# Performance work log

Hardware: AMD Instinct MI355X
Metric: run time of the kernel (lower is better)

## Reference

```python
import jax, jax.numpy as jnp
import numpy as np

N_QUBITS = 10
N_LAYERS = 3
OUT_MIN, OUT_MAX = -0.1, 0.1


def _apply_1q(state, U, wire):
    # state: (B, 2**n) complex64; U: (2,2) complex64 gate on `wire` (wire 0 = MSB, PennyLane order)
    B = state.shape[0]
    s = state.reshape(B, 2 ** wire, 2, -1)
    s = jnp.einsum('ij,bljr->blir', U, s)
    return s.reshape(B, -1)


def _apply_ry_batched(state, theta, wire):
    # per-sample RY(theta) on `wire`; theta: (B,)
    B = state.shape[0]
    s = state.reshape(B, 2 ** wire, 2, -1)
    c = jnp.cos(0.5 * theta)[:, None, None]
    si = jnp.sin(0.5 * theta)[:, None, None]
    a0, a1 = s[:, :, 0, :], s[:, :, 1, :]
    s = jnp.stack([c * a0 - si * a1, si * a0 + c * a1], axis=2)
    return s.reshape(B, -1)


def _apply_cnot(state, ctrl):
    # CNOT with control=ctrl, target=ctrl+1 (adjacent wires)
    B = state.shape[0]
    s = state.reshape(B, 2 ** ctrl, 2, 2, -1)
    s = jnp.stack([s[:, :, 0], s[:, :, 1, ::-1]], axis=2)
    return s.reshape(B, -1)


def _circuit(z, weights):
    # Faithful statevector simulation of the PennyLane qnode, batched over samples.
    B = z.shape[0]
    n = N_QUBITS
    state = jnp.zeros((B, 2 ** n), jnp.complex64).at[:, 0].set(1.0)
    zc = jnp.clip(z, -1.0, 1.0)
    for i in range(n):
        state = _apply_ry_batched(state, zc[:, i % zc.shape[1]], i)
    # Fuse RZ(a)->RY(b)->RZ(c) per (layer, qubit) into one 2x2 unitary: U = Rz(c) @ Ry(b) @ Rz(a)
    a, b, c = weights[..., 0], weights[..., 1], weights[..., 2]
    ea, eap = jnp.exp(-0.5j * a), jnp.exp(0.5j * a)
    ec, ecp = jnp.exp(-0.5j * c), jnp.exp(0.5j * c)
    cb, sb = jnp.cos(0.5 * b), jnp.sin(0.5 * b)
    U = jnp.stack([jnp.stack([ec * cb * ea, -ec * sb * eap], -1),
                   jnp.stack([ecp * sb * ea, ecp * cb * eap], -1)], -2)  # (L, Q, 2, 2)
    U = U.astype(jnp.complex64)
    for l in range(N_LAYERS):
        for i in range(n):
            state = _apply_1q(state, U[l, i], i)
        for i in range(n - 1):
            state = _apply_cnot(state, i)
    probs = jnp.abs(state) ** 2  # (B, 2**n) float32
    feats = []
    for i in range(n):
        p = probs.reshape(B, 2 ** i, 2, -1)
        feats.append(p[:, :, 0].sum((1, 2)) - p[:, :, 1].sum((1, 2)))  # <Z_i>
    return jnp.stack(feats, -1)  # (B, n_qubits)


def setup_inputs() -> dict:
    key = jax.random.key(0)
    ks = jax.random.split(key, 8)
    B = 4096
    return {
        'z': jax.random.normal(ks[0], (B, N_QUBITS), jnp.float32),
        'weights': jax.random.normal(ks[1], (N_LAYERS, N_QUBITS, 3), jnp.float32) * 0.01,
        'W1': jax.random.normal(ks[2], (N_QUBITS, 32), jnp.float32) * 0.3,
        'b1': jax.random.normal(ks[3], (32,), jnp.float32) * 0.05,
        'W2': jax.random.normal(ks[4], (32, 16), jnp.float32) * 0.2,
        'b2': jax.random.normal(ks[5], (16,), jnp.float32) * 0.05,
        'W3': jax.random.normal(ks[6], (16, 1), jnp.float32) * 0.2,
        'b3': jax.random.normal(ks[7], (1,), jnp.float32) * 0.05,
    }


def reference(z, weights, W1, b1, W2, b2, W3, b3):
    feats = _circuit(z, weights)                  # (B, n_qubits)
    h = jnp.tanh(feats @ W1 + b1)
    h = jnp.tanh(h @ W2 + b2)
    raw = h @ W3 + b3                             # (B, 1)
    return jax.nn.sigmoid(raw) * (OUT_MAX - OUT_MIN) + OUT_MIN
```

## Files before the change

kernel.cpp:

```cpp
#include <hip/hip_runtime.h>

namespace {

constexpr int NQ = 10;

struct cplx { float re, im; };

__device__ __forceinline__ cplx cmul(cplx a, cplx b) {
  return cplx{ fmaf(a.re, b.re, -a.im * b.im), fmaf(a.re, b.im, a.im * b.re) };
}
__device__ __forceinline__ cplx cmadd2(cplx u, cplx a, cplx v, cplx b) {
  cplx r;
  r.re = fmaf(u.re, a.re, fmaf(-u.im, a.im, fmaf(v.re, b.re, -v.im * b.im)));
  r.im = fmaf(u.re, a.im, fmaf( u.im, a.re, fmaf(v.re, b.im,  v.im * b.re)));
  return r;
}
__device__ __forceinline__ cplx csel(bool c, cplx x, cplx y) {
  return cplx{ c ? x.re : y.re, c ? x.im : y.im };
}

__device__ __forceinline__ float fast_tanh(float x) {
  float xc = fminf(fmaxf(x, -10.f), 10.f);
  float e = __expf(2.f * xc);
  return __fdividef(e - 1.f, e + 1.f);
}

__device__ __forceinline__ float rdlane(float v, int l) {
  return __int_as_float(__builtin_amdgcn_readlane(__float_as_int(v), l));
}
template<int CTRL>
__device__ __forceinline__ float dppf(float v) {
  return __int_as_float(__builtin_amdgcn_update_dpp(0, __float_as_int(v), CTRL, 0xF, 0xF, true));
}
template<int CTRL>
__device__ __forceinline__ cplx dppc(cplx v) { return cplx{ dppf<CTRL>(v.re), dppf<CTRL>(v.im) }; }

template<int PAT>
__device__ __forceinline__ float swzf(float v) {
  return __int_as_float(__builtin_amdgcn_ds_swizzle(__float_as_int(v), PAT));
}
__device__ __forceinline__ float bperm(int addr, float v) {
  return __int_as_float(__builtin_amdgcn_ds_bpermute(addr, __float_as_int(v)));
}

struct Umat { float r00,i00,r01,i01,r10,i10,r11,i11; };
__device__ __forceinline__ void getU(const Umat& m, int g,
                                     cplx& u00, cplx& u01, cplx& u10, cplx& u11) {
  u00 = cplx{rdlane(m.r00, g), rdlane(m.i00, g)};
  u01 = cplx{rdlane(m.r01, g), rdlane(m.i01, g)};
  u10 = cplx{rdlane(m.r10, g), rdlane(m.i10, g)};
  u11 = cplx{rdlane(m.r11, g), rdlane(m.i11, g)};
}

__device__ __forceinline__ void gate_lane_rt(cplx (&amp)[16], int lane, const Umat& m,
                                             int g, int LX, int HIL) {
  cplx u00, u01, u10, u11; getU(m, g, u00, u01, u10, u11);
  bool hi = (__popc(lane & HIL) & 1) != 0;
  cplx cA = csel(hi, u11, u00), cB = csel(hi, u10, u01);
  const int addr = (lane ^ LX) << 2;
  float ore[16], oim[16];
  #pragma unroll
  for (int t = 0; t < 16; ++t) { ore[t] = bperm(addr, amp[t].re); oim[t] = bperm(addr, amp[t].im); }
  #pragma unroll
  for (int t = 0; t < 16; ++t) amp[t] = cmadd2(cA, amp[t], cB, cplx{ore[t], oim[t]});
}

template<int CTRL, int LOCX, int HIL>
__device__ __forceinline__ void gate_mixed(cplx (&amp)[16], int lane, cplx u00,cplx u01,cplx u10,cplx u11) {
  bool hi = (__popc(lane & HIL) & 1) != 0;
  cplx cA = csel(hi, u11, u00), cB = csel(hi, u10, u01);
  #pragma unroll
  for (int t0 = 0; t0 < 16; ++t0) {
    if (t0 & LOCX) continue;
    const int t1 = t0 | LOCX;
    cplx o0 = dppc<CTRL>(amp[t1]);
    cplx o1 = dppc<CTRL>(amp[t0]);
    amp[t0] = cmadd2(cA, amp[t0], cB, o0);
    amp[t1] = cmadd2(cA, amp[t1], cB, o1);
  }
}
constexpr int hbit(int m) { return m >= 8 ? 8 : (m >= 4 ? 4 : (m >= 2 ? 2 : 1)); }
template<int PLOC, int HIL, int HILOC>
__device__ __forceinline__ void gate_local(cplx (&amp)[16], int lane, cplx u00,cplx u01,cplx u10,cplx u11) {
  bool h0 = (__popc(lane & HIL) & 1) != 0;
  cplx cA0 = csel(h0, u11, u00), cB0 = csel(h0, u10, u01);
  cplx cA1 = csel(h0, u00, u11), cB1 = csel(h0, u01, u10);
  #pragma unroll
  for (int ta = 0; ta < 16; ++ta) {
    if (ta & hbit(PLOC)) continue;
    const int tb = ta ^ PLOC;
    const bool pa = (__popc(ta & HILOC) & 1) != 0;
    cplx aA = amp[ta], aB = amp[tb];
    if (!pa) { amp[ta] = cmadd2(cA0, aA, cB0, aB); amp[tb] = cmadd2(cA1, aB, cB1, aA); }
    else     { amp[ta] = cmadd2(cA1, aA, cB1, aB); amp[tb] = cmadd2(cA0, aB, cB0, aA); }
  }
}

__device__ __forceinline__ float wht6(float v, float s1, float s2, float s4,
                                      float s8, float s16, float s32) {
  float o;
  o = dppf<0xB1>(v);               v = fmaf(s1,  v, o);
  o = dppf<0x4E>(v);               v = fmaf(s2,  v, o);
  o = dppf<0x1B>(dppf<0x141>(v));  v = fmaf(s4,  v, o);
  o = dppf<0x128>(v);              v = fmaf(s8,  v, o);
  o = swzf<0x401F>(v);             v = fmaf(s16, v, o);
  o = __shfl_xor(v, 32);           v = fmaf(s32, v, o);
  return v;
}

constexpr int pk6(int a, int b, int c, int d, int e) {
  return a | (b << 6) | (c << 12) | (d << 18) | (e << 24);
}
constexpr int LX1  = pk6(0x30, 0x18, 0x0C, 0x06, 0x03);
constexpr int HIL1 = pk6(0x20, 0x30, 0x38, 0x3C, 0x3E);
constexpr int LX2  = pk6(0x28, 0x14, 0x0A, 0x05, 0);
constexpr int HIL2 = pk6(0x20, 0x10, 0x28, 0x14, 0);

__global__ __launch_bounds__(64, 1)
void qgan_kernel(const float* __restrict__ z, const float* __restrict__ wts,
                 const float* __restrict__ W1, const float* __restrict__ b1,
                 const float* __restrict__ W2, const float* __restrict__ b2,
                 const float* __restrict__ W3, const float* __restrict__ b3,
                 float* __restrict__ out, int B)
{
  const int lane = threadIdx.x;
  const int wv   = blockIdx.x;
  if (wv >= B) return;

  const int j32 = lane & 31, k16 = lane & 15;
  float w1r[10];
  #pragma unroll
  for (int i = 0; i < NQ; ++i) w1r[i] = W1[i * 32 + j32];
  float b1v = b1[j32], b2v = b2[k16], w3v = W3[k16], b3v = b3[0];

  Umat m;
  {
    int g = (lane < 30) ? lane : 0;
    float wa = wts[g * 3 + 0], wb = wts[g * 3 + 1], wc = wts[g * 3 + 2];
    float al = 0.5f * (wa + wc), be = 0.5f * (wa - wc), hb = 0.5f * wb;
    float ca = __cosf(al),  sa = __sinf(al);
    float cbe = __cosf(be), sbe = __sinf(be);
    float cb = __cosf(hb),  sb = __sinf(hb);
    m.r00 =  cb * ca;  m.i00 = -cb * sa;
    m.r01 = -sb * cbe; m.i01 = -sb * sbe;
    m.r10 =  sb * cbe; m.i10 = -sb * sbe;
    m.r11 =  cb * ca;  m.i11 =  cb * sa;
  }

  cplx u00, u01, u10, u11;
  const float* zp = z + wv * NQ;

  cplx laneF = {1.f, 0.f};
  #pragma unroll
  for (int q = 0; q < 6; ++q) {
    float zz = fminf(fmaxf(zp[q], -1.f), 1.f);
    float c0 = __cosf(0.5f * zz), s0 = __sinf(0.5f * zz);
    getU(m, q, u00, u01, u10, u11);
    cplx va = { fmaf(u00.re, c0, u01.re * s0), fmaf(u00.im, c0, u01.im * s0) };
    cplx vb = { fmaf(u10.re, c0, u11.re * s0), fmaf(u10.im, c0, u11.im * s0) };
    cplx f = csel((lane >> (5 - q)) & 1, vb, va);
    laneF = (q == 0) ? f : cmul(laneF, f);
  }
  cplx va_[4], vb_[4];
  #pragma unroll
  for (int q = 6; q < 10; ++q) {
    float zz = fminf(fmaxf(zp[q], -1.f), 1.f);
    float c0 = __cosf(0.5f * zz), s0 = __sinf(0.5f * zz);
    getU(m, q, u00, u01, u10, u11);
    va_[q - 6] = { fmaf(u00.re, c0, u01.re * s0), fmaf(u00.im, c0, u01.im * s0) };
    vb_[q - 6] = { fmaf(u10.re, c0, u11.re * s0), fmaf(u10.im, c0, u11.im * s0) };
  }

  cplx amp[16];
  {
    cplx P2[4];
    P2[0] = cmul(va_[2], va_[3]);
    P2[1] = cmul(va_[2], vb_[3]);
    P2[2] = cmul(vb_[2], va_[3]);
    P2[3] = cmul(vb_[2], vb_[3]);
    cplx g0 = cmul(laneF, va_[0]);
    cplx g1 = cmul(laneF, vb_[0]);
    #pragma unroll
    for (int t = 0; t < 16; ++t) {
      cplx t7 = ((t >> 2) & 1) ? vb_[1] : va_[1];
      cplx tt = cmul(t7, P2[t & 3]);
      amp[t] = cmul(((t >> 3) & 1) ? g1 : g0, tt);
    }
  }

  #pragma unroll 1
  for (int i = 0; i < 5; ++i)
    gate_lane_rt(amp, lane, m, 10 + i, (LX1 >> (6 * i)) & 63, (HIL1 >> (6 * i)) & 63);
  getU(m, 15, u00,u01,u10,u11); gate_mixed<0xB1, 8, 0x3F>(amp, lane, u00,u01,u10,u11);
  getU(m, 16, u00,u01,u10,u11); gate_local<0xC, 0x3F, 0x8>(amp, lane, u00,u01,u10,u11);
  getU(m, 17, u00,u01,u10,u11); gate_local<0x6, 0x3F, 0xC>(amp, lane, u00,u01,u10,u11);
  getU(m, 18, u00,u01,u10,u11); gate_local<0x3, 0x3F, 0xE>(amp, lane, u00,u01,u10,u11);
  getU(m, 19, u00,u01,u10,u11); gate_local<0x1, 0x3F, 0xF>(amp, lane, u00,u01,u10,u11);

  #pragma unroll 1
  for (int i = 0; i < 4; ++i)
    gate_lane_rt(amp, lane, m, 20 + i, (LX2 >> (6 * i)) & 63, (HIL2 >> (6 * i)) & 63);
  getU(m, 24, u00,u01,u10,u11); gate_mixed<0x4E, 8, 0x2A>(amp, lane, u00,u01,u10,u11);
  getU(m, 25, u00,u01,u10,u11); gate_mixed<0xB1, 4, 0x15>(amp, lane, u00,u01,u10,u11);
  getU(m, 26, u00,u01,u10,u11); gate_local<0xA, 0x2A, 0x8>(amp, lane, u00,u01,u10,u11);
  getU(m, 27, u00,u01,u10,u11); gate_local<0x5, 0x15, 0x4>(amp, lane, u00,u01,u10,u11);
  getU(m, 28, u00,u01,u10,u11); gate_local<0x2, 0x2A, 0xA>(amp, lane, u00,u01,u10,u11);
  getU(m, 29, u00,u01,u10,u11); gate_local<0x1, 0x15, 0x5>(amp, lane, u00,u01,u10,u11);

  float p[16];
  #pragma unroll
  for (int t = 0; t < 16; ++t)
    p[t] = fmaf(amp[t].re, amp[t].re, amp[t].im * amp[t].im);

  #pragma unroll
  for (int k = 1; k <= 8; k <<= 1) {
    #pragma unroll
    for (int t = 0; t < 16; ++t) {
      if (t & k) continue;
      float a = p[t], b = p[t | k];
      p[t] = a + b; p[t | k] = a - b;
    }
  }

  float w2r[32];
  #pragma unroll
  for (int jj = 0; jj < 32; ++jj) w2r[jj] = W2[jj * 16 + k16];

  float s1  = (lane & 1)  ? -1.f : 1.f;
  float s2  = (lane & 2)  ? -1.f : 1.f;
  float s4  = (lane & 4)  ? -1.f : 1.f;
  float s8  = (lane & 8)  ? -1.f : 1.f;
  float s16 = (lane & 16) ? -1.f : 1.f;
  float s32 = (lane & 32) ? -1.f : 1.f;
  float B0 = wht6(p[0],   s1,s2,s4,s8,s16,s32);
  float B8 = wht6(p[8],   s1,s2,s4,s8,s16,s32);
  float BC = wht6(p[0xC], s1,s2,s4,s8,s16,s32);
  float B6 = wht6(p[6],   s1,s2,s4,s8,s16,s32);
  float B3 = wht6(p[3],   s1,s2,s4,s8,s16,s32);

  float feats[10];
  feats[0] = rdlane(B0, 0x20); feats[1] = rdlane(B0, 0x30);
  feats[2] = rdlane(B0, 0x18); feats[3] = rdlane(B0, 0x0C);
  feats[4] = rdlane(B0, 0x26); feats[5] = rdlane(B0, 0x33);
  feats[6] = rdlane(B8, 0x19); feats[7] = rdlane(BC, 0x0C);
  feats[8] = rdlane(B6, 0x26); feats[9] = rdlane(B3, 0x33);

  float acc = b1v;
  #pragma unroll
  for (int i = 0; i < NQ; ++i) acc = fmaf(feats[i], w1r[i], acc);
  float h1 = fast_tanh(acc);

  float acc2 = b2v;
  #pragma unroll
  for (int jj = 0; jj < 32; ++jj)
    acc2 = fmaf(rdlane(h1, jj), w2r[jj], acc2);
  float h2 = fast_tanh(acc2);

  float vv = h2 * w3v;
  vv += dppf<0xB1>(vv);
  vv += dppf<0x4E>(vv);
  vv += dppf<0x1B>(dppf<0x141>(vv));
  vv += dppf<0x128>(vv);

  if (lane == 0) out[wv] = 0.1f * fast_tanh(0.5f * (vv + b3v));
}

}

extern "C" void kernel_launch(void* const* d_in, const int* in_sizes, int n_in,
                              void* d_out, int out_size, void* d_ws, size_t ws_size,
                              hipStream_t stream) {
  const float* z   = (const float*)d_in[0];
  const float* wts = (const float*)d_in[1];
  const float* W1  = (const float*)d_in[2];
  const float* b1  = (const float*)d_in[3];
  const float* W2  = (const float*)d_in[4];
  const float* b2  = (const float*)d_in[5];
  const float* W3  = (const float*)d_in[6];
  const float* b3  = (const float*)d_in[7];
  float* out = (float*)d_out;
  (void)d_ws; (void)ws_size;

  int B = in_sizes[0] / NQ;
  hipLaunchKernelGGL(qgan_kernel, dim3(B), dim3(64), 0, stream,
                     z, wts, W1, b1, W2, b2, W3, b3, out, B);
}
```

Baseline: 90.94 us.

## Apply CNOT chains explicitly via bpermute and pack four waves per block

Replaces the earlier approach, which folded the CNOT chains into permuted gate indexing with parity selects, with an explicit CNOT-chain permutation per layer done through one bpermute pass plus a register reshuffle. Single-qubit gates become simple per-bit lane gates and local gates with no parity bookkeeping. The launch moves from one 64-thread block per sample to 256-thread blocks holding four samples, and the MLP weight loads are moved later to lower register pressure. This adds three cross-lane permutation passes but simplifies every gate and aims to improve occupancy and scheduling.

```diff
diff --git a/kernel.cpp b/kernel.cpp
--- a/kernel.cpp
+++ b/kernel.cpp
@@ -32,9 +32,6 @@
 __device__ __forceinline__ float dppf(float v) {
   return __int_as_float(__builtin_amdgcn_update_dpp(0, __float_as_int(v), CTRL, 0xF, 0xF, true));
 }
-template<int CTRL>
-__device__ __forceinline__ cplx dppc(cplx v) { return cplx{ dppf<CTRL>(v.re), dppf<CTRL>(v.im) }; }
-
 template<int PAT>
 __device__ __forceinline__ float swzf(float v) {
   return __int_as_float(__builtin_amdgcn_ds_swizzle(__float_as_int(v), PAT));
@@ -52,12 +49,12 @@
   u11 = cplx{rdlane(m.r11, g), rdlane(m.i11, g)};
 }
 
-__device__ __forceinline__ void gate_lane_rt(cplx (&amp)[16], int lane, const Umat& m,
-                                             int g, int LX, int HIL) {
+__device__ __forceinline__ void lane_gate(cplx (&amp)[16], int lane, const Umat& m,
+                                          int g, int kb) {
   cplx u00, u01, u10, u11; getU(m, g, u00, u01, u10, u11);
-  bool hi = (__popc(lane & HIL) & 1) != 0;
+  bool hi = ((lane >> kb) & 1) != 0;
   cplx cA = csel(hi, u11, u00), cB = csel(hi, u10, u01);
-  const int addr = (lane ^ LX) << 2;
+  const int addr = (lane ^ (1 << kb)) << 2;
   float ore[16], oim[16];
   #pragma unroll
   for (int t = 0; t < 16; ++t) { ore[t] = bperm(addr, amp[t].re); oim[t] = bperm(addr, amp[t].im); }
@@ -65,34 +62,31 @@
   for (int t = 0; t < 16; ++t) amp[t] = cmadd2(cA, amp[t], cB, cplx{ore[t], oim[t]});
 }
 
-template<int CTRL, int LOCX, int HIL>
-__device__ __forceinline__ void gate_mixed(cplx (&amp)[16], int lane, cplx u00,cplx u01,cplx u10,cplx u11) {
-  bool hi = (__popc(lane & HIL) & 1) != 0;
-  cplx cA = csel(hi, u11, u00), cB = csel(hi, u10, u01);
+template<int BBIT>
+__device__ __forceinline__ void local_gate(cplx (&amp)[16], const Umat& m, int g) {
+  cplx u00, u01, u10, u11; getU(m, g, u00, u01, u10, u11);
   #pragma unroll
   for (int t0 = 0; t0 < 16; ++t0) {
-    if (t0 & LOCX) continue;
-    const int t1 = t0 | LOCX;
-    cplx o0 = dppc<CTRL>(amp[t1]);
-    cplx o1 = dppc<CTRL>(amp[t0]);
-    amp[t0] = cmadd2(cA, amp[t0], cB, o0);
-    amp[t1] = cmadd2(cA, amp[t1], cB, o1);
-  }
-}
-constexpr int hbit(int m) { return m >= 8 ? 8 : (m >= 4 ? 4 : (m >= 2 ? 2 : 1)); }
-template<int PLOC, int HIL, int HILOC>
-__device__ __forceinline__ void gate_local(cplx (&amp)[16], int lane, cplx u00,cplx u01,cplx u10,cplx u11) {
-  bool h0 = (__popc(lane & HIL) & 1) != 0;
-  cplx cA0 = csel(h0, u11, u00), cB0 = csel(h0, u10, u01);
-  cplx cA1 = csel(h0, u00, u11), cB1 = csel(h0, u01, u10);
-  #pragma unroll
-  for (int ta = 0; ta < 16; ++ta) {
-    if (ta & hbit(PLOC)) continue;
-    const int tb = ta ^ PLOC;
-    const bool pa = (__popc(ta & HILOC) & 1) != 0;
-    cplx aA = amp[ta], aB = amp[tb];
-    if (!pa) { amp[ta] = cmadd2(cA0, aA, cB0, aB); amp[tb] = cmadd2(cA1, aB, cB1, aA); }
-    else     { amp[ta] = cmadd2(cA1, aA, cB1, aB); amp[tb] = cmadd2(cA0, aB, cB0, aA); }
+    if (t0 & BBIT) continue;
+    const int t1 = t0 | BBIT;
+    cplx a0 = amp[t0], a1 = amp[t1];
+    amp[t0] = cmadd2(u00, a0, u01, a1);
+    amp[t1] = cmadd2(u10, a0, u11, a1);
+  }
+}
+
+__device__ __forceinline__ void chain(cplx (&amp)[16], int lane) {
+  const int addr = ((lane ^ (lane >> 1)) & 63) << 2;
+  float ore[16], oim[16];
+  #pragma unroll
+  for (int t = 0; t < 16; ++t) { ore[t] = bperm(addr, amp[t].re); oim[t] = bperm(addr, amp[t].im); }
+  const bool ctrl = (lane & 1) != 0;
+  #pragma unroll
+  for (int t = 0; t < 16; ++t) {
+    const int ta = t ^ (t >> 1);
+    const int tb = ta ^ 8;
+    amp[t].re = ctrl ? ore[tb] : ore[ta];
+    amp[t].im = ctrl ? oim[tb] : oim[ta];
   }
 }
 
@@ -108,30 +102,17 @@
   return v;
 }
 
-constexpr int pk6(int a, int b, int c, int d, int e) {
-  return a | (b << 6) | (c << 12) | (d << 18) | (e << 24);
-}
-constexpr int LX1  = pk6(0x30, 0x18, 0x0C, 0x06, 0x03);
-constexpr int HIL1 = pk6(0x20, 0x30, 0x38, 0x3C, 0x3E);
-constexpr int LX2  = pk6(0x28, 0x14, 0x0A, 0x05, 0);
-constexpr int HIL2 = pk6(0x20, 0x10, 0x28, 0x14, 0);
-
-__global__ __launch_bounds__(64, 1)
+__global__ __launch_bounds__(256, 4)
 void qgan_kernel(const float* __restrict__ z, const float* __restrict__ wts,
                  const float* __restrict__ W1, const float* __restrict__ b1,
                  const float* __restrict__ W2, const float* __restrict__ b2,
                  const float* __restrict__ W3, const float* __restrict__ b3,
                  float* __restrict__ out, int B)
 {
-  const int lane = threadIdx.x;
-  const int wv   = blockIdx.x;
+  const int tid  = blockIdx.x * 256 + threadIdx.x;
+  const int lane = threadIdx.x & 63;
+  const int wv   = __builtin_amdgcn_readfirstlane(tid >> 6);
   if (wv >= B) return;
-
-  const int j32 = lane & 31, k16 = lane & 15;
-  float w1r[10];
-  #pragma unroll
-  for (int i = 0; i < NQ; ++i) w1r[i] = W1[i * 32 + j32];
-  float b1v = b1[j32], b2v = b2[k16], w3v = W3[k16], b3v = b3[0];
 
   Umat m;
   {
@@ -189,23 +170,19 @@
   }
 
   #pragma unroll 1
-  for (int i = 0; i < 5; ++i)
-    gate_lane_rt(amp, lane, m, 10 + i, (LX1 >> (6 * i)) & 63, (HIL1 >> (6 * i)) & 63);
-  getU(m, 15, u00,u01,u10,u11); gate_mixed<0xB1, 8, 0x3F>(amp, lane, u00,u01,u10,u11);
-  getU(m, 16, u00,u01,u10,u11); gate_local<0xC, 0x3F, 0x8>(amp, lane, u00,u01,u10,u11);
-  getU(m, 17, u00,u01,u10,u11); gate_local<0x6, 0x3F, 0xC>(amp, lane, u00,u01,u10,u11);
-  getU(m, 18, u00,u01,u10,u11); gate_local<0x3, 0x3F, 0xE>(amp, lane, u00,u01,u10,u11);
-  getU(m, 19, u00,u01,u10,u11); gate_local<0x1, 0x3F, 0xF>(amp, lane, u00,u01,u10,u11);
-
-  #pragma unroll 1
-  for (int i = 0; i < 4; ++i)
-    gate_lane_rt(amp, lane, m, 20 + i, (LX2 >> (6 * i)) & 63, (HIL2 >> (6 * i)) & 63);
-  getU(m, 24, u00,u01,u10,u11); gate_mixed<0x4E, 8, 0x2A>(amp, lane, u00,u01,u10,u11);
-  getU(m, 25, u00,u01,u10,u11); gate_mixed<0xB1, 4, 0x15>(amp, lane, u00,u01,u10,u11);
-  getU(m, 26, u00,u01,u10,u11); gate_local<0xA, 0x2A, 0x8>(amp, lane, u00,u01,u10,u11);
-  getU(m, 27, u00,u01,u10,u11); gate_local<0x5, 0x15, 0x4>(amp, lane, u00,u01,u10,u11);
-  getU(m, 28, u00,u01,u10,u11); gate_local<0x2, 0x2A, 0xA>(amp, lane, u00,u01,u10,u11);
-  getU(m, 29, u00,u01,u10,u11); gate_local<0x1, 0x15, 0x5>(amp, lane, u00,u01,u10,u11);
+  for (int l = 0; l < 3; ++l) {
+    if (l) {
+      const int gbase = 10 * l;
+      #pragma unroll 1
+      for (int q = 0; q < 6; ++q)
+        lane_gate(amp, lane, m, gbase + q, 5 - q);
+      local_gate<8>(amp, m, gbase + 6);
+      local_gate<4>(amp, m, gbase + 7);
+      local_gate<2>(amp, m, gbase + 8);
+      local_gate<1>(amp, m, gbase + 9);
+    }
+    chain(amp, lane);
+  }
 
   float p[16];
   #pragma unroll
@@ -222,47 +199,44 @@
     }
   }
 
-  float w2r[32];
-  #pragma unroll
-  for (int jj = 0; jj < 32; ++jj) w2r[jj] = W2[jj * 16 + k16];
-
   float s1  = (lane & 1)  ? -1.f : 1.f;
   float s2  = (lane & 2)  ? -1.f : 1.f;
   float s4  = (lane & 4)  ? -1.f : 1.f;
   float s8  = (lane & 8)  ? -1.f : 1.f;
   float s16 = (lane & 16) ? -1.f : 1.f;
   float s32 = (lane & 32) ? -1.f : 1.f;
-  float B0 = wht6(p[0],   s1,s2,s4,s8,s16,s32);
-  float B8 = wht6(p[8],   s1,s2,s4,s8,s16,s32);
-  float BC = wht6(p[0xC], s1,s2,s4,s8,s16,s32);
-  float B6 = wht6(p[6],   s1,s2,s4,s8,s16,s32);
-  float B3 = wht6(p[3],   s1,s2,s4,s8,s16,s32);
+  float B0 = wht6(p[0], s1,s2,s4,s8,s16,s32);
+  float B8 = wht6(p[8], s1,s2,s4,s8,s16,s32);
+  float B4 = wht6(p[4], s1,s2,s4,s8,s16,s32);
+  float B2 = wht6(p[2], s1,s2,s4,s8,s16,s32);
+  float B1 = wht6(p[1], s1,s2,s4,s8,s16,s32);
 
   float feats[10];
-  feats[0] = rdlane(B0, 0x20); feats[1] = rdlane(B0, 0x30);
-  feats[2] = rdlane(B0, 0x18); feats[3] = rdlane(B0, 0x0C);
-  feats[4] = rdlane(B0, 0x26); feats[5] = rdlane(B0, 0x33);
-  feats[6] = rdlane(B8, 0x19); feats[7] = rdlane(BC, 0x0C);
-  feats[8] = rdlane(B6, 0x26); feats[9] = rdlane(B3, 0x33);
-
-  float acc = b1v;
-  #pragma unroll
-  for (int i = 0; i < NQ; ++i) acc = fmaf(feats[i], w1r[i], acc);
+  feats[0] = rdlane(B0, 0x20); feats[1] = rdlane(B0, 0x10);
+  feats[2] = rdlane(B0, 0x08); feats[3] = rdlane(B0, 0x04);
+  feats[4] = rdlane(B0, 0x02); feats[5] = rdlane(B0, 0x01);
+  feats[6] = rdlane(B8, 0);    feats[7] = rdlane(B4, 0);
+  feats[8] = rdlane(B2, 0);    feats[9] = rdlane(B1, 0);
+
+  const int j32 = lane & 31, k16 = lane & 15;
+  float acc = b1[j32];
+  #pragma unroll
+  for (int i = 0; i < NQ; ++i) acc = fmaf(feats[i], W1[i * 32 + j32], acc);
   float h1 = fast_tanh(acc);
 
-  float acc2 = b2v;
+  float acc2 = b2[k16];
   #pragma unroll
   for (int jj = 0; jj < 32; ++jj)
-    acc2 = fmaf(rdlane(h1, jj), w2r[jj], acc2);
+    acc2 = fmaf(rdlane(h1, jj), W2[jj * 16 + k16], acc2);
   float h2 = fast_tanh(acc2);
 
-  float vv = h2 * w3v;
+  float vv = h2 * W3[k16];
   vv += dppf<0xB1>(vv);
   vv += dppf<0x4E>(vv);
   vv += dppf<0x1B>(dppf<0x141>(vv));
   vv += dppf<0x128>(vv);
 
-  if (lane == 0) out[wv] = 0.1f * fast_tanh(0.5f * (vv + b3v));
+  if (lane == 0) out[wv] = 0.1f * fast_tanh(0.5f * (vv + b3[0]));
 }
 
 }
@@ -282,6 +256,7 @@
   (void)d_ws; (void)ws_size;
 
   int B = in_sizes[0] / NQ;
-  hipLaunchKernelGGL(qgan_kernel, dim3(B), dim3(64), 0, stream,
+  int blocks = (B + 3) / 4;
+  hipLaunchKernelGGL(qgan_kernel, dim3(blocks), dim3(256), 0, stream,
                      z, wts, W1, b1, W2, b2, W3, b3, out, B);
 }
```

Measured after the change: 104.0 us. 14.4% more time.

## Process two samples per wavefront and replace bpermute exchanges with DPP/swizzle

Applied to the files above, without the earlier changes.

Each wavefront now simulates two batch samples at once, which halves the block count and amortises the per-block setup (weight loads, gate-matrix trig, readlane broadcasts) across two states while giving more independent instructions to interleave. Most cross-lane gate exchanges that previously went through ds_bpermute now use DPP or ds_swizzle patterns, and only the xor-0x30 and xor-0x28 cases still use bpermute. The runtime-looped lane gates are fully unrolled with compile-time patterns. The cost is roughly double the register use for amplitudes, and odd B would read and write past the end of the arrays.

```diff
diff --git a/kernel.cpp b/kernel.cpp
--- a/kernel.cpp
+++ b/kernel.cpp
@@ -34,11 +34,14 @@
 }
 template<int CTRL>
 __device__ __forceinline__ cplx dppc(cplx v) { return cplx{ dppf<CTRL>(v.re), dppf<CTRL>(v.im) }; }
-
+template<int C1, int C2>
+__device__ __forceinline__ cplx dppc2(cplx v) { return dppc<C2>(dppc<C1>(v)); }
 template<int PAT>
 __device__ __forceinline__ float swzf(float v) {
   return __int_as_float(__builtin_amdgcn_ds_swizzle(__float_as_int(v), PAT));
 }
+template<int PAT>
+__device__ __forceinline__ cplx swzc(cplx v) { return cplx{ swzf<PAT>(v.re), swzf<PAT>(v.im) }; }
 __device__ __forceinline__ float bperm(int addr, float v) {
   return __int_as_float(__builtin_amdgcn_ds_bpermute(addr, __float_as_int(v)));
 }
@@ -52,48 +55,61 @@
   u11 = cplx{rdlane(m.r11, g), rdlane(m.i11, g)};
 }
 
-__device__ __forceinline__ void gate_lane_rt(cplx (&amp)[16], int lane, const Umat& m,
-                                             int g, int LX, int HIL) {
-  cplx u00, u01, u10, u11; getU(m, g, u00, u01, u10, u11);
+template<int HIL>
+__device__ __forceinline__ void coeffs(int lane, cplx u00, cplx u01, cplx u10, cplx u11,
+                                       cplx& cA, cplx& cB) {
   bool hi = (__popc(lane & HIL) & 1) != 0;
-  cplx cA = csel(hi, u11, u00), cB = csel(hi, u10, u01);
-  const int addr = (lane ^ LX) << 2;
-  float ore[16], oim[16];
-  #pragma unroll
-  for (int t = 0; t < 16; ++t) { ore[t] = bperm(addr, amp[t].re); oim[t] = bperm(addr, amp[t].im); }
-  #pragma unroll
-  for (int t = 0; t < 16; ++t) amp[t] = cmadd2(cA, amp[t], cB, cplx{ore[t], oim[t]});
-}
-
-template<int CTRL, int LOCX, int HIL>
-__device__ __forceinline__ void gate_mixed(cplx (&amp)[16], int lane, cplx u00,cplx u01,cplx u10,cplx u11) {
-  bool hi = (__popc(lane & HIL) & 1) != 0;
-  cplx cA = csel(hi, u11, u00), cB = csel(hi, u10, u01);
-  #pragma unroll
-  for (int t0 = 0; t0 < 16; ++t0) {
-    if (t0 & LOCX) continue;
-    const int t1 = t0 | LOCX;
-    cplx o0 = dppc<CTRL>(amp[t1]);
-    cplx o1 = dppc<CTRL>(amp[t0]);
-    amp[t0] = cmadd2(cA, amp[t0], cB, o0);
-    amp[t1] = cmadd2(cA, amp[t1], cB, o1);
-  }
-}
+  cA = csel(hi, u11, u00); cB = csel(hi, u10, u01);
+}
+
+template<int HIL, class X>
+__device__ __forceinline__ void lane_gate2(cplx (&amp)[2][16], int lane,
+    cplx u00, cplx u01, cplx u10, cplx u11, X xch) {
+  cplx cA, cB; coeffs<HIL>(lane, u00,u01,u10,u11, cA, cB);
+  cplx o[2][16];
+  #pragma unroll
+  for (int e = 0; e < 2; ++e)
+    #pragma unroll
+    for (int t = 0; t < 16; ++t) o[e][t] = xch(amp[e][t]);
+  #pragma unroll
+  for (int e = 0; e < 2; ++e)
+    #pragma unroll
+    for (int t = 0; t < 16; ++t) amp[e][t] = cmadd2(cA, amp[e][t], cB, o[e][t]);
+}
+
+template<int LOCX, int HIL, class X>
+__device__ __forceinline__ void mixed_gate2(cplx (&amp)[2][16], int lane,
+    cplx u00, cplx u01, cplx u10, cplx u11, X xch) {
+  cplx cA, cB; coeffs<HIL>(lane, u00,u01,u10,u11, cA, cB);
+  cplx o[2][16];
+  #pragma unroll
+  for (int e = 0; e < 2; ++e)
+    #pragma unroll
+    for (int t = 0; t < 16; ++t) o[e][t] = xch(amp[e][t ^ LOCX]);
+  #pragma unroll
+  for (int e = 0; e < 2; ++e)
+    #pragma unroll
+    for (int t = 0; t < 16; ++t) amp[e][t] = cmadd2(cA, amp[e][t], cB, o[e][t]);
+}
+
 constexpr int hbit(int m) { return m >= 8 ? 8 : (m >= 4 ? 4 : (m >= 2 ? 2 : 1)); }
 template<int PLOC, int HIL, int HILOC>
-__device__ __forceinline__ void gate_local(cplx (&amp)[16], int lane, cplx u00,cplx u01,cplx u10,cplx u11) {
+__device__ __forceinline__ void local_gate2(cplx (&amp)[2][16], int lane,
+    cplx u00, cplx u01, cplx u10, cplx u11) {
   bool h0 = (__popc(lane & HIL) & 1) != 0;
   cplx cA0 = csel(h0, u11, u00), cB0 = csel(h0, u10, u01);
   cplx cA1 = csel(h0, u00, u11), cB1 = csel(h0, u01, u10);
   #pragma unroll
-  for (int ta = 0; ta < 16; ++ta) {
-    if (ta & hbit(PLOC)) continue;
-    const int tb = ta ^ PLOC;
-    const bool pa = (__popc(ta & HILOC) & 1) != 0;
-    cplx aA = amp[ta], aB = amp[tb];
-    if (!pa) { amp[ta] = cmadd2(cA0, aA, cB0, aB); amp[tb] = cmadd2(cA1, aB, cB1, aA); }
-    else     { amp[ta] = cmadd2(cA1, aA, cB1, aB); amp[tb] = cmadd2(cA0, aB, cB0, aA); }
-  }
+  for (int e = 0; e < 2; ++e)
+    #pragma unroll
+    for (int ta = 0; ta < 16; ++ta) {
+      if (ta & hbit(PLOC)) continue;
+      const int tb = ta ^ PLOC;
+      const bool pa = (__popc(ta & HILOC) & 1) != 0;
+      cplx aA = amp[e][ta], aB = amp[e][tb];
+      if (!pa) { amp[e][ta] = cmadd2(cA0, aA, cB0, aB); amp[e][tb] = cmadd2(cA1, aB, cB1, aA); }
+      else     { amp[e][ta] = cmadd2(cA1, aA, cB1, aB); amp[e][tb] = cmadd2(cA0, aB, cB0, aA); }
+    }
 }
 
 __device__ __forceinline__ float wht6(float v, float s1, float s2, float s4,
@@ -108,14 +124,6 @@
   return v;
 }
 
-constexpr int pk6(int a, int b, int c, int d, int e) {
-  return a | (b << 6) | (c << 12) | (d << 18) | (e << 24);
-}
-constexpr int LX1  = pk6(0x30, 0x18, 0x0C, 0x06, 0x03);
-constexpr int HIL1 = pk6(0x20, 0x30, 0x38, 0x3C, 0x3E);
-constexpr int LX2  = pk6(0x28, 0x14, 0x0A, 0x05, 0);
-constexpr int HIL2 = pk6(0x20, 0x10, 0x28, 0x14, 0);
-
 __global__ __launch_bounds__(64, 1)
 void qgan_kernel(const float* __restrict__ z, const float* __restrict__ wts,
                  const float* __restrict__ W1, const float* __restrict__ b1,
@@ -124,8 +132,8 @@
                  float* __restrict__ out, int B)
 {
   const int lane = threadIdx.x;
-  const int wv   = blockIdx.x;
-  if (wv >= B) return;
+  const int e0   = blockIdx.x * 2;
+  if (e0 >= B) return;
 
   const int j32 = lane & 31, k16 = lane & 15;
   float w1r[10];
@@ -148,83 +156,89 @@
   }
 
   cplx u00, u01, u10, u11;
-  const float* zp = z + wv * NQ;
-
-  cplx laneF = {1.f, 0.f};
-  #pragma unroll
-  for (int q = 0; q < 6; ++q) {
-    float zz = fminf(fmaxf(zp[q], -1.f), 1.f);
-    float c0 = __cosf(0.5f * zz), s0 = __sinf(0.5f * zz);
-    getU(m, q, u00, u01, u10, u11);
-    cplx va = { fmaf(u00.re, c0, u01.re * s0), fmaf(u00.im, c0, u01.im * s0) };
-    cplx vb = { fmaf(u10.re, c0, u11.re * s0), fmaf(u10.im, c0, u11.im * s0) };
-    cplx f = csel((lane >> (5 - q)) & 1, vb, va);
-    laneF = (q == 0) ? f : cmul(laneF, f);
+  const float* zp[2] = { z + e0 * NQ, z + (e0 + 1) * NQ };
+
+  cplx amp[2][16];
+  {
+    cplx laneF[2] = { {1.f, 0.f}, {1.f, 0.f} };
+    #pragma unroll
+    for (int q = 0; q < 6; ++q) {
+      getU(m, q, u00, u01, u10, u11);
+      #pragma unroll
+      for (int e = 0; e < 2; ++e) {
+        float zz = fminf(fmaxf(zp[e][q], -1.f), 1.f);
+        float c0 = __cosf(0.5f * zz), s0 = __sinf(0.5f * zz);
+        cplx va = { fmaf(u00.re, c0, u01.re * s0), fmaf(u00.im, c0, u01.im * s0) };
+        cplx vb = { fmaf(u10.re, c0, u11.re * s0), fmaf(u10.im, c0, u11.im * s0) };
+        cplx f = csel((lane >> (5 - q)) & 1, vb, va);
+        laneF[e] = (q == 0) ? f : cmul(laneF[e], f);
+      }
+    }
+    cplx va_[2][4], vb_[2][4];
+    #pragma unroll
+    for (int q = 6; q < 10; ++q) {
+      getU(m, q, u00, u01, u10, u11);
+      #pragma unroll
+      for (int e = 0; e < 2; ++e) {
+        float zz = fminf(fmaxf(zp[e][q], -1.f), 1.f);
+        float c0 = __cosf(0.5f * zz), s0 = __sinf(0.5f * zz);
+        va_[e][q - 6] = { fmaf(u00.re, c0, u01.re * s0), fmaf(u00.im, c0, u01.im * s0) };
+        vb_[e][q - 6] = { fmaf(u10.re, c0, u11.re * s0), fmaf(u10.im, c0, u11.im * s0) };
+      }
+    }
+    #pragma unroll
+    for (int e = 0; e < 2; ++e) {
+      cplx P2[4];
+      P2[0] = cmul(va_[e][2], va_[e][3]);
+      P2[1] = cmul(va_[e][2], vb_[e][3]);
+      P2[2] = cmul(vb_[e][2], va_[e][3]);
+      P2[3] = cmul(vb_[e][2], vb_[e][3]);
+      cplx g0 = cmul(laneF[e], va_[e][0]);
+      cplx g1 = cmul(laneF[e], vb_[e][0]);
+      #pragma unroll
+      for (int t = 0; t < 16; ++t) {
+        cplx t7 = ((t >> 2) & 1) ? vb_[e][1] : va_[e][1];
+        cplx tt = cmul(t7, P2[t & 3]);
+        amp[e][t] = cmul(((t >> 3) & 1) ? g1 : g0, tt);
+      }
+    }
   }
-  cplx va_[4], vb_[4];
-  #pragma unroll
-  for (int q = 6; q < 10; ++q) {
-    float zz = fminf(fmaxf(zp[q], -1.f), 1.f);
-    float c0 = __cosf(0.5f * zz), s0 = __sinf(0.5f * zz);
-    getU(m, q, u00, u01, u10, u11);
-    va_[q - 6] = { fmaf(u00.re, c0, u01.re * s0), fmaf(u00.im, c0, u01.im * s0) };
-    vb_[q - 6] = { fmaf(u10.re, c0, u11.re * s0), fmaf(u10.im, c0, u11.im * s0) };
-  }
-
-  cplx amp[16];
-  {
-    cplx P2[4];
-    P2[0] = cmul(va_[2], va_[3]);
-    P2[1] = cmul(va_[2], vb_[3]);
-    P2[2] = cmul(vb_[2], va_[3]);
-    P2[3] = cmul(vb_[2], vb_[3]);
-    cplx g0 = cmul(laneF, va_[0]);
-    cplx g1 = cmul(laneF, vb_[0]);
-    #pragma unroll
-    for (int t = 0; t < 16; ++t) {
-      cplx t7 = ((t >> 2) & 1) ? vb_[1] : va_[1];
-      cplx tt = cmul(t7, P2[t & 3]);
-      amp[t] = cmul(((t >> 3) & 1) ? g1 : g0, tt);
-    }
-  }
-
-  #pragma unroll 1
-  for (int i = 0; i < 5; ++i)
-    gate_lane_rt(amp, lane, m, 10 + i, (LX1 >> (6 * i)) & 63, (HIL1 >> (6 * i)) & 63);
-  getU(m, 15, u00,u01,u10,u11); gate_mixed<0xB1, 8, 0x3F>(amp, lane, u00,u01,u10,u11);
-  getU(m, 16, u00,u01,u10,u11); gate_local<0xC, 0x3F, 0x8>(amp, lane, u00,u01,u10,u11);
-  getU(m, 17, u00,u01,u10,u11); gate_local<0x6, 0x3F, 0xC>(amp, lane, u00,u01,u10,u11);
-  getU(m, 18, u00,u01,u10,u11); gate_local<0x3, 0x3F, 0xE>(amp, lane, u00,u01,u10,u11);
-  getU(m, 19, u00,u01,u10,u11); gate_local<0x1, 0x3F, 0xF>(amp, lane, u00,u01,u10,u11);
-
-  #pragma unroll 1
-  for (int i = 0; i < 4; ++i)
-    gate_lane_rt(amp, lane, m, 20 + i, (LX2 >> (6 * i)) & 63, (HIL2 >> (6 * i)) & 63);
-  getU(m, 24, u00,u01,u10,u11); gate_mixed<0x4E, 8, 0x2A>(amp, lane, u00,u01,u10,u11);
-  getU(m, 25, u00,u01,u10,u11); gate_mixed<0xB1, 4, 0x15>(amp, lane, u00,u01,u10,u11);
-  getU(m, 26, u00,u01,u10,u11); gate_local<0xA, 0x2A, 0x8>(amp, lane, u00,u01,u10,u11);
-  getU(m, 27, u00,u01,u10,u11); gate_local<0x5, 0x15, 0x4>(amp, lane, u00,u01,u10,u11);
-  getU(m, 28, u00,u01,u10,u11); gate_local<0x2, 0x2A, 0xA>(amp, lane, u00,u01,u10,u11);
-  getU(m, 29, u00,u01,u10,u11); gate_local<0x1, 0x15, 0x5>(amp, lane, u00,u01,u10,u11);
-
-  float p[16];
-  #pragma unroll
-  for (int t = 0; t < 16; ++t)
-    p[t] = fmaf(amp[t].re, amp[t].re, amp[t].im * amp[t].im);
-
-  #pragma unroll
-  for (int k = 1; k <= 8; k <<= 1) {
-    #pragma unroll
-    for (int t = 0; t < 16; ++t) {
-      if (t & k) continue;
-      float a = p[t], b = p[t | k];
-      p[t] = a + b; p[t | k] = a - b;
-    }
-  }
-
-  float w2r[32];
-  #pragma unroll
-  for (int jj = 0; jj < 32; ++jj) w2r[jj] = W2[jj * 16 + k16];
+
+  const int a1 = ((lane ^ 0x30) & 63) << 2;
+  const int a2 = ((lane ^ 0x28) & 63) << 2;
+  auto xb1  = [&](cplx v) { return cplx{ bperm(a1, v.re), bperm(a1, v.im) }; };
+  auto xb2  = [&](cplx v) { return cplx{ bperm(a2, v.re), bperm(a2, v.im) }; };
+  auto xs18 = [ ](cplx v) { return swzc<0x601F>(v); };
+  auto xs14 = [ ](cplx v) { return swzc<0x501F>(v); };
+  auto xdC  = [ ](cplx v) { return dppc2<0x140, 0x1B>(v); };
+  auto xd6  = [ ](cplx v) { return dppc2<0x141, 0xB1>(v); };
+  auto xd3  = [ ](cplx v) { return dppc<0x1B>(v); };
+  auto xdA  = [ ](cplx v) { return dppc2<0x128, 0x4E>(v); };
+  auto xd5  = [ ](cplx v) { return dppc2<0x141, 0x4E>(v); };
+  auto xd2  = [ ](cplx v) { return dppc<0x4E>(v); };
+  auto xd1  = [ ](cplx v) { return dppc<0xB1>(v); };
+
+  getU(m, 10, u00,u01,u10,u11); lane_gate2<0x20>(amp, lane, u00,u01,u10,u11, xb1);
+  getU(m, 11, u00,u01,u10,u11); lane_gate2<0x30>(amp, lane, u00,u01,u10,u11, xs18);
+  getU(m, 12, u00,u01,u10,u11); lane_gate2<0x38>(amp, lane, u00,u01,u10,u11, xdC);
+  getU(m, 13, u00,u01,u10,u11); lane_gate2<0x3C>(amp, lane, u00,u01,u10,u11, xd6);
+  getU(m, 14, u00,u01,u10,u11); lane_gate2<0x3E>(amp, lane, u00,u01,u10,u11, xd3);
+  getU(m, 15, u00,u01,u10,u11); mixed_gate2<8, 0x3F>(amp, lane, u00,u01,u10,u11, xd1);
+  getU(m, 16, u00,u01,u10,u11); local_gate2<0xC, 0x3F, 0x8>(amp, lane, u00,u01,u10,u11);
+  getU(m, 17, u00,u01,u10,u11); local_gate2<0x6, 0x3F, 0xC>(amp, lane, u00,u01,u10,u11);
+  getU(m, 18, u00,u01,u10,u11); local_gate2<0x3, 0x3F, 0xE>(amp, lane, u00,u01,u10,u11);
+  getU(m, 19, u00,u01,u10,u11); local_gate2<0x1, 0x3F, 0xF>(amp, lane, u00,u01,u10,u11);
+
+  getU(m, 20, u00,u01,u10,u11); lane_gate2<0x20>(amp, lane, u00,u01,u10,u11, xb2);
+  getU(m, 21, u00,u01,u10,u11); lane_gate2<0x10>(amp, lane, u00,u01,u10,u11, xs14);
+  getU(m, 22, u00,u01,u10,u11); lane_gate2<0x28>(amp, lane, u00,u01,u10,u11, xdA);
+  getU(m, 23, u00,u01,u10,u11); lane_gate2<0x14>(amp, lane, u00,u01,u10,u11, xd5);
+  getU(m, 24, u00,u01,u10,u11); mixed_gate2<8, 0x2A>(amp, lane, u00,u01,u10,u11, xd2);
+  getU(m, 25, u00,u01,u10,u11); mixed_gate2<4, 0x15>(amp, lane, u00,u01,u10,u11, xd1);
+  getU(m, 26, u00,u01,u10,u11); local_gate2<0xA, 0x2A, 0x8>(amp, lane, u00,u01,u10,u11);
+  getU(m, 27, u00,u01,u10,u11); local_gate2<0x5, 0x15, 0x4>(amp, lane, u00,u01,u10,u11);
+  getU(m, 28, u00,u01,u10,u11); local_gate2<0x2, 0x2A, 0xA>(amp, lane, u00,u01,u10,u11);
+  getU(m, 29, u00,u01,u10,u11); local_gate2<0x1, 0x15, 0x5>(amp, lane, u00,u01,u10,u11);
 
   float s1  = (lane & 1)  ? -1.f : 1.f;
   float s2  = (lane & 2)  ? -1.f : 1.f;
@@ -232,37 +246,62 @@
   float s8  = (lane & 8)  ? -1.f : 1.f;
   float s16 = (lane & 16) ? -1.f : 1.f;
   float s32 = (lane & 32) ? -1.f : 1.f;
-  float B0 = wht6(p[0],   s1,s2,s4,s8,s16,s32);
-  float B8 = wht6(p[8],   s1,s2,s4,s8,s16,s32);
-  float BC = wht6(p[0xC], s1,s2,s4,s8,s16,s32);
-  float B6 = wht6(p[6],   s1,s2,s4,s8,s16,s32);
-  float B3 = wht6(p[3],   s1,s2,s4,s8,s16,s32);
-
-  float feats[10];
-  feats[0] = rdlane(B0, 0x20); feats[1] = rdlane(B0, 0x30);
-  feats[2] = rdlane(B0, 0x18); feats[3] = rdlane(B0, 0x0C);
-  feats[4] = rdlane(B0, 0x26); feats[5] = rdlane(B0, 0x33);
-  feats[6] = rdlane(B8, 0x19); feats[7] = rdlane(BC, 0x0C);
-  feats[8] = rdlane(B6, 0x26); feats[9] = rdlane(B3, 0x33);
-
-  float acc = b1v;
-  #pragma unroll
-  for (int i = 0; i < NQ; ++i) acc = fmaf(feats[i], w1r[i], acc);
-  float h1 = fast_tanh(acc);
-
-  float acc2 = b2v;
-  #pragma unroll
-  for (int jj = 0; jj < 32; ++jj)
-    acc2 = fmaf(rdlane(h1, jj), w2r[jj], acc2);
-  float h2 = fast_tanh(acc2);
-
-  float vv = h2 * w3v;
-  vv += dppf<0xB1>(vv);
-  vv += dppf<0x4E>(vv);
-  vv += dppf<0x1B>(dppf<0x141>(vv));
-  vv += dppf<0x128>(vv);
-
-  if (lane == 0) out[wv] = 0.1f * fast_tanh(0.5f * (vv + b3v));
+
+  float feats[2][10];
+  #pragma unroll
+  for (int e = 0; e < 2; ++e) {
+    float p[16];
+    #pragma unroll
+    for (int t = 0; t < 16; ++t)
+      p[t] = fmaf(amp[e][t].re, amp[e][t].re, amp[e][t].im * amp[e][t].im);
+    #pragma unroll
+    for (int k = 1; k <= 8; k <<= 1) {
+      #pragma unroll
+      for (int t = 0; t < 16; ++t) {
+        if (t & k) continue;
+        float a = p[t], b = p[t | k];
+        p[t] = a + b; p[t | k] = a - b;
+      }
+    }
+    float B0 = wht6(p[0],   s1,s2,s4,s8,s16,s32);
+    float B8 = wht6(p[8],   s1,s2,s4,s8,s16,s32);
+    float BC = wht6(p[0xC], s1,s2,s4,s8,s16,s32);
+    float B6 = wht6(p[6],   s1,s2,s4,s8,s16,s32);
+    float B3 = wht6(p[3],   s1,s2,s4,s8,s16,s32);
+    feats[e][0] = rdlane(B0, 0x20); feats[e][1] = rdlane(B0, 0x30);
+    feats[e][2] = rdlane(B0, 0x18); feats[e][3] = rdlane(B0, 0x0C);
+    feats[e][4] = rdlane(B0, 0x26); feats[e][5] = rdlane(B0, 0x33);
+    feats[e][6] = rdlane(B8, 0x19); feats[e][7] = rdlane(BC, 0x0C);
+    feats[e][8] = rdlane(B6, 0x26); feats[e][9] = rdlane(B3, 0x33);
+  }
+
+  float w2r[32];
+  #pragma unroll
+  for (int jj = 0; jj < 32; ++jj) w2r[jj] = W2[jj * 16 + k16];
+
+  float r[2];
+  #pragma unroll
+  for (int e = 0; e < 2; ++e) {
+    float acc = b1v;
+    #pragma unroll
+    for (int i = 0; i < NQ; ++i) acc = fmaf(feats[e][i], w1r[i], acc);
+    float h1 = fast_tanh(acc);
+
+    float acc2 = b2v;
+    #pragma unroll
+    for (int jj = 0; jj < 32; ++jj)
+      acc2 = fmaf(rdlane(h1, jj), w2r[jj], acc2);
+    float h2 = fast_tanh(acc2);
+
+    float vv = h2 * w3v;
+    vv += dppf<0xB1>(vv);
+    vv += dppf<0x4E>(vv);
+    vv += dppf<0x1B>(dppf<0x141>(vv));
+    vv += dppf<0x128>(vv);
+    r[e] = 0.1f * fast_tanh(0.5f * (vv + b3v));
+  }
+
+  if (lane == 0) { out[e0] = r[0]; out[e0 + 1] = r[1]; }
 }
 
 }
@@ -282,6 +321,7 @@
   (void)d_ws; (void)ws_size;
 
   int B = in_sizes[0] / NQ;
-  hipLaunchKernelGGL(qgan_kernel, dim3(B), dim3(64), 0, stream,
+  int blocks = (B + 1) / 2;
+  hipLaunchKernelGGL(qgan_kernel, dim3(blocks), dim3(64), 0, stream,
                      z, wts, W1, b1, W2, b2, W3, b3, out, B);
 }
```

Result: slower. 94.11 us (+3.5%).
